# Optimization experiments

Measured on AMD Instinct MI355X. Metric: run time of the kernel, lower is better.

Reference implementation:

```python
import jax, jax.numpy as jnp
import numpy as np


def setup_inputs() -> dict:
    key = jax.random.key(0)
    k1, k2 = jax.random.split(key)
    # [B, C=1, D, H, W] single-channel 3D volume
    x = jax.random.normal(k1, (8, 1, 128, 128, 128), dtype=jnp.float32)
    # 3x3x3 finite-difference stencil weights (frozen parameter in the original)
    kernel = jax.random.normal(k2, (3, 3, 3), dtype=jnp.float32)
    return {"x": x, "kernel": kernel}


def reference(x, kernel):
    # F.pad(..., 'circular') with pad=1 on each spatial side -> wrap-around pad
    xp = jnp.pad(x, ((0, 0), (0, 0), (1, 1), (1, 1), (1, 1)), mode='wrap')
    # kernel.reshape(1, 1, 3, 3, 3): out_ch=1, in_ch=1 (OIDHW)
    k = kernel.reshape(1, 1, 3, 3, 3)
    # F.conv3d(padding='valid') == cross-correlation, matches lax conv semantics
    out = jax.lax.conv_general_dilated(
        xp, k,
        window_strides=(1, 1, 1),
        padding='VALID',
        dimension_numbers=('NCDHW', 'OIDHW', 'NCDHW'),
    )
    return out  # [8, 1, 128, 128, 128]
```

## Files before the change

### kernel.cpp

```cpp
#include <hip/hip_runtime.h>

#define DIM   128
#define PLANE (DIM*DIM)
#define TD    16

typedef float vfloat4 __attribute__((ext_vector_type(4)));

__global__ __launch_bounds__(256, 2)
void conv3d_circ_rp2(
    const float* __restrict__ x, const float* __restrict__ kern,
    float* __restrict__ out)
{
    const int tid = threadIdx.x;
    const int bid = blockIdx.x;
    const int b  = bid >> 6;
    const int ht = (bid >> 3) & 7;
    const int dt = bid & 7;
    const int h0 = ht * 16;
    const int d0 = dt * TD;

    const int wq   = (tid & 31) * 4;
    const int hg   = h0 + (tid >> 5) * 2;
    const int lane = tid & 63;
    const int lleft  = (lane & 32) | ((lane - 1) & 31);
    const int lright = (lane & 32) | ((lane + 1) & 31);

    const int ro[4] = {((hg - 1) & (DIM - 1)) * DIM + wq,
                       hg * DIM + wq,
                       ((hg + 1) & (DIM - 1)) * DIM + wq,
                       ((hg + 2) & (DIM - 1)) * DIM + wq};

    float K0[9], K1[9], K2[9];
#pragma unroll
    for (int i = 0; i < 9; ++i) { K0[i] = kern[i]; K1[i] = kern[9 + i]; K2[i] = kern[18 + i]; }

    const float* xb = x + (size_t)b * (DIM * PLANE);
    float* ob = out + (size_t)b * (DIM * PLANE) + (size_t)hg * DIM + wq;

    float rA[4][4], rB[4][4], rC[4][4];
    float accA[2][4], accB[2][4];
#pragma unroll
    for (int r = 0; r < 2; ++r)
#pragma unroll
        for (int j = 0; j < 4; ++j) { accA[r][j] = 0.f; accB[r][j] = 0.f; }

#define LOAD(R, P)                                                            \
    {                                                                         \
        const float* xp = xb + (size_t)(((P) & (DIM - 1)) * PLANE);           \
        _Pragma("unroll") for (int rr = 0; rr < 4; ++rr) {                    \
            const vfloat4 a = *(const vfloat4*)(xp + ro[rr]);                 \
            R[rr][0] = a.x; R[rr][1] = a.y; R[rr][2] = a.z; R[rr][3] = a.w;   \
        }                                                                     \
    }

#define STEP(RC_, RN_, I, DOLOAD)                                             \
    {                                                                         \
        const int p = d0 - 1 + (I);                                           \
        if (DOLOAD) LOAD(RN_, p + 2);                                         \
        float e[4][6];                                                        \
        _Pragma("unroll") for (int rr = 0; rr < 4; ++rr) {                    \
            e[rr][0] = __shfl(RC_[rr][3], lleft);                \
            e[rr][1] = RC_[rr][0]; e[rr][2] = RC_[rr][1];                     \
            e[rr][3] = RC_[rr][2]; e[rr][4] = RC_[rr][3];                     \
            e[rr][5] = __shfl(RC_[rr][0], lright);               \
        }                                                                     \
        float c0[2][4];                                                       \
        _Pragma("unroll") for (int r = 0; r < 2; ++r)                         \
        _Pragma("unroll") for (int j = 0; j < 4; ++j) c0[r][j] = 0.f;         \
        _Pragma("unroll") for (int ch = 0; ch < 3; ++ch)                      \
        _Pragma("unroll") for (int cw = 0; cw < 3; ++cw) {                    \
            const float k0 = K0[ch * 3 + cw];                                 \
            const float k1 = K1[ch * 3 + cw];                                 \
            const float k2 = K2[ch * 3 + cw];                                 \
            _Pragma("unroll") for (int r = 0; r < 2; ++r)                     \
            _Pragma("unroll") for (int j = 0; j < 4; ++j) {                   \
                const float xv = e[r + ch][j + cw];                           \
                accA[r][j] = fmaf(k2, xv, accA[r][j]);                        \
                accB[r][j] = fmaf(k1, xv, accB[r][j]);                        \
                c0[r][j]   = fmaf(k0, xv, c0[r][j]);                          \
            }                                                                 \
        }                                                                     \
        if ((I) >= 2) {                                                       \
            float* op = ob + (size_t)(p - 1) * PLANE;                         \
            _Pragma("unroll") for (int r = 0; r < 2; ++r) {                   \
                vfloat4 v;                                                    \
                v.x = accA[r][0]; v.y = accA[r][1];                           \
                v.z = accA[r][2]; v.w = accA[r][3];                           \
                __builtin_nontemporal_store(v, (vfloat4*)(op + r * DIM));     \
            }                                                                 \
        }                                                                     \
        _Pragma("unroll") for (int r = 0; r < 2; ++r)                        \
        _Pragma("unroll") for (int j = 0; j < 4; ++j)                         \
            { accA[r][j] = accB[r][j]; accB[r][j] = c0[r][j]; }               \
    }

    LOAD(rA, d0 - 1);
    LOAD(rB, d0);

#pragma unroll 1
    for (int i = 0; i < 15; i += 3) {
        STEP(rA, rC, i + 0, true);
        STEP(rB, rA, i + 1, true);
        STEP(rC, rB, i + 2, true);
    }
    STEP(rA, rC, 15, true);
    STEP(rB, rA, 16, false);
    STEP(rC, rB, 17, false);
#undef STEP
#undef LOAD
}

extern "C" void kernel_launch(void* const* d_in, const int* in_sizes, int n_in,
                              void* d_out, int out_size, void* d_ws, size_t ws_size,
                              hipStream_t stream) {
    const float* x    = (const float*)d_in[0];
    const float* kern = (const float*)d_in[1];
    float*       out  = (float*)d_out;
    conv3d_circ_rp2<<<dim3(512), dim3(256), 0, stream>>>(x, kern, out);
}
```

Before: 28.19 us.

## Rotate accumulators as a ring, double-buffer input planes, fully unroll depth loop

```diff
diff --git a/kernel.cpp b/kernel.cpp
--- a/kernel.cpp
+++ b/kernel.cpp
@@ -6,8 +6,7 @@
 
 typedef float vfloat4 __attribute__((ext_vector_type(4)));
 
-__global__ __launch_bounds__(256, 2)
-void conv3d_circ_rp2(
+__global__ __launch_bounds__(256, 4) void conv3d_circ_ring(
     const float* __restrict__ x, const float* __restrict__ kern,
     float* __restrict__ out)
 {
@@ -37,12 +36,12 @@
     const float* xb = x + (size_t)b * (DIM * PLANE);
     float* ob = out + (size_t)b * (DIM * PLANE) + (size_t)hg * DIM + wq;
 
-    float rA[4][4], rB[4][4], rC[4][4];
-    float accA[2][4], accB[2][4];
+    float rA[4][4], rB[4][4];
+    float a0[2][4], a1[2][4], a2[2][4];
 #pragma unroll
     for (int r = 0; r < 2; ++r)
 #pragma unroll
-        for (int j = 0; j < 4; ++j) { accA[r][j] = 0.f; accB[r][j] = 0.f; }
+        for (int j = 0; j < 4; ++j) { a1[r][j] = 0.f; a2[r][j] = 0.f; }
 
 #define LOAD(R, P)                                                            \
     {                                                                         \
@@ -53,10 +52,10 @@
         }                                                                     \
     }
 
-#define STEP(RC_, RN_, I, DOLOAD)                                             \
+#define STEP(RC_, RN_, AX, AY, AZ, I, DOLOAD, DOSTORE)                        \
     {                                                                         \
         const int p = d0 - 1 + (I);                                           \
-        if (DOLOAD) LOAD(RN_, p + 2);                                         \
+        if (DOLOAD) LOAD(RN_, p + 1);                                         \
         float e[4][6];                                                        \
         _Pragma("unroll") for (int rr = 0; rr < 4; ++rr) {                    \
             e[rr][0] = __shfl(RC_[rr][3], lleft);                \
@@ -64,9 +63,6 @@
             e[rr][3] = RC_[rr][2]; e[rr][4] = RC_[rr][3];                     \
             e[rr][5] = __shfl(RC_[rr][0], lright);               \
         }                                                                     \
-        float c0[2][4];                                                       \
-        _Pragma("unroll") for (int r = 0; r < 2; ++r)                         \
-        _Pragma("unroll") for (int j = 0; j < 4; ++j) c0[r][j] = 0.f;         \
         _Pragma("unroll") for (int ch = 0; ch < 3; ++ch)                      \
         _Pragma("unroll") for (int cw = 0; cw < 3; ++cw) {                    \
             const float k0 = K0[ch * 3 + cw];                                 \
@@ -75,37 +71,43 @@
             _Pragma("unroll") for (int r = 0; r < 2; ++r)                     \
             _Pragma("unroll") for (int j = 0; j < 4; ++j) {                   \
                 const float xv = e[r + ch][j + cw];                           \
-                accA[r][j] = fmaf(k2, xv, accA[r][j]);                        \
-                accB[r][j] = fmaf(k1, xv, accB[r][j]);                        \
-                c0[r][j]   = fmaf(k0, xv, c0[r][j]);                          \
+                AX[r][j] = fmaf(k2, xv, AX[r][j]);                            \
+                AY[r][j] = fmaf(k1, xv, AY[r][j]);                            \
+                if (ch == 0 && cw == 0) AZ[r][j] = k0 * xv;                   \
+                else                    AZ[r][j] = fmaf(k0, xv, AZ[r][j]);    \
             }                                                                 \
         }                                                                     \
-        if ((I) >= 2) {                                                       \
+        if (DOSTORE) {                                                        \
             float* op = ob + (size_t)(p - 1) * PLANE;                         \
             _Pragma("unroll") for (int r = 0; r < 2; ++r) {                   \
                 vfloat4 v;                                                    \
-                v.x = accA[r][0]; v.y = accA[r][1];                           \
-                v.z = accA[r][2]; v.w = accA[r][3];                           \
+                v.x = AX[r][0]; v.y = AX[r][1];                               \
+                v.z = AX[r][2]; v.w = AX[r][3];                               \
                 __builtin_nontemporal_store(v, (vfloat4*)(op + r * DIM));     \
             }                                                                 \
         }                                                                     \
-        _Pragma("unroll") for (int r = 0; r < 2; ++r)                        \
-        _Pragma("unroll") for (int j = 0; j < 4; ++j)                         \
-            { accA[r][j] = accB[r][j]; accB[r][j] = c0[r][j]; }               \
     }
 
     LOAD(rA, d0 - 1);
-    LOAD(rB, d0);
 
-#pragma unroll 1
-    for (int i = 0; i < 15; i += 3) {
-        STEP(rA, rC, i + 0, true);
-        STEP(rB, rA, i + 1, true);
-        STEP(rC, rB, i + 2, true);
-    }
-    STEP(rA, rC, 15, true);
-    STEP(rB, rA, 16, false);
-    STEP(rC, rB, 17, false);
+    STEP(rA, rB, a1, a2, a0,  0, true,  false);
+    STEP(rB, rA, a2, a0, a1,  1, true,  false);
+    STEP(rA, rB, a0, a1, a2,  2, true,  true );
+    STEP(rB, rA, a1, a2, a0,  3, true,  true );
+    STEP(rA, rB, a2, a0, a1,  4, true,  true );
+    STEP(rB, rA, a0, a1, a2,  5, true,  true );
+    STEP(rA, rB, a1, a2, a0,  6, true,  true );
+    STEP(rB, rA, a2, a0, a1,  7, true,  true );
+    STEP(rA, rB, a0, a1, a2,  8, true,  true );
+    STEP(rB, rA, a1, a2, a0,  9, true,  true );
+    STEP(rA, rB, a2, a0, a1, 10, true,  true );
+    STEP(rB, rA, a0, a1, a2, 11, true,  true );
+    STEP(rA, rB, a1, a2, a0, 12, true,  true );
+    STEP(rB, rA, a2, a0, a1, 13, true,  true );
+    STEP(rA, rB, a0, a1, a2, 14, true,  true );
+    STEP(rB, rA, a1, a2, a0, 15, true,  true );
+    STEP(rA, rB, a2, a0, a1, 16, true,  true );
+    STEP(rB, rA, a0, a1, a2, 17, false, true );
 #undef STEP
 #undef LOAD
 }
@@ -116,5 +118,5 @@
     const float* x    = (const float*)d_in[0];
     const float* kern = (const float*)d_in[1];
     float*       out  = (float*)d_out;
-    conv3d_circ_rp2<<<dim3(512), dim3(256), 0, stream>>>(x, kern, out);
+    conv3d_circ_ring<<<dim3(512), dim3(256), 0, stream>>>(x, kern, out);
 }
```

After: 28.06 us. Within noise of the previous version (-0.5%).
